# Kernel optimization log

Hardware: AMD Instinct MI355X
Metric: run time of the kernel (lower is better)

Reference implementation:

```python
import jax, jax.numpy as jnp
import numpy as np

IN_F = 2048
OUT_F = 2048
BATCH = 16384
BASE_SPARSITY = 0.02
REVIVAL_DENSITY = 0.2   # rows for dead ('low') output neurons
RELIEF_DENSITY = 0.15   # cols for saturated ('high') input neurons
DEAD = np.arange(16)                      # 'low' extrema (row indices)
SATURATED = np.arange(100, 900, 100)      # 'high' extrema (col indices)


def _make_mask(key):
    k1, k2, k3 = jax.random.split(key, 3)
    base = (jax.random.uniform(k1, (OUT_F, IN_F)) < BASE_SPARSITY).astype(jnp.float32)
    patch = jnp.zeros((OUT_F, IN_F), jnp.float32)
    # dense-ish rows for dead output neurons
    row_patch = (jax.random.uniform(k2, (len(DEAD), IN_F)) < REVIVAL_DENSITY).astype(jnp.float32)
    patch = patch.at[jnp.asarray(DEAD), :].set(row_patch)
    # dense-ish cols for saturated input neurons (overwrite, matching torch order)
    col_patch = (jax.random.uniform(k3, (OUT_F, len(SATURATED))) < RELIEF_DENSITY).astype(jnp.float32)
    patch = patch.at[:, jnp.asarray(SATURATED)].set(col_patch)
    return jnp.maximum(base, patch)


def setup_inputs() -> dict:
    key = jax.random.key(0)
    kx, kw, km = jax.random.split(key, 3)
    x = jax.random.normal(kx, (BATCH, IN_F), dtype=jnp.float32)
    # kaiming_uniform_(a=sqrt(5)) -> U(-bound, bound), bound = sqrt(6/((1+a^2)*fan_in)) = 1/sqrt(fan_in)
    bound = 1.0 / np.sqrt(IN_F)
    weight = jax.random.uniform(kw, (OUT_F, IN_F), minval=-bound, maxval=bound, dtype=jnp.float32)
    bias = jnp.zeros((OUT_F,), jnp.float32)
    mask = _make_mask(km)
    return {"x": x, "weight": weight, "bias": bias, "mask": mask}


def reference(x, weight, bias, mask):
    # F.linear(x, weight * mask, bias): y = x @ (W*M)^T + b
    return jnp.einsum('bi,oi->bo', x, weight * mask) + bias
```

## Files before the change

### kernel.cpp

```cpp
#include <hip/hip_runtime.h>
#include <stdint.h>

#define BATCH 16384
#define IN_F 2048
#define OUT_F 2048

typedef unsigned short u16;
typedef __attribute__((ext_vector_type(8))) short bf16x8;
typedef __attribute__((ext_vector_type(4))) float f32x4;

__device__ __forceinline__ u16 f2bf(float f) {
  union { float f; uint32_t u; } v; v.f = f;
  uint32_t u = v.u;
  u += 0x7FFFu + ((u >> 16) & 1u);
  return (u16)(u >> 16);
}


__global__ void cvt_fused(const float4* __restrict__ x, const float4* __restrict__ w,
                          const float4* __restrict__ m, u16* __restrict__ xb,
                          u16* __restrict__ wb) {
  const int NX = BATCH * IN_F / 4;
  int i = blockIdx.x * 256 + threadIdx.x;
  if (i < NX) {
    float4 v = x[i];
    uint2 p;
    p.x = (uint32_t)f2bf(v.x) | ((uint32_t)f2bf(v.y) << 16);
    p.y = (uint32_t)f2bf(v.z) | ((uint32_t)f2bf(v.w) << 16);
    ((uint2*)xb)[i] = p;
  } else {
    int j = i - NX;
    float4 wv = w[j];
    float4 mv = m[j];
    uint2 p;
    p.x = (uint32_t)f2bf(wv.x * mv.x) | ((uint32_t)f2bf(wv.y * mv.y) << 16);
    p.y = (uint32_t)f2bf(wv.z * mv.z) | ((uint32_t)f2bf(wv.w * mv.w) << 16);
    ((uint2*)wb)[j] = p;
  }
}


__device__ __forceinline__ void async_cp16(const void* g, void* l) {
  __builtin_amdgcn_global_load_lds(
      (const __attribute__((address_space(1))) void*)g,
      (__attribute__((address_space(3))) void*)l,
      16, 0, 0);
}


#define BK 32
#define NT (IN_F / BK)

__global__ __launch_bounds__(512, 2) void gemm_bf16(const u16* __restrict__ A,
                                                    const u16* __restrict__ B,
                                                    const float* __restrict__ bias,
                                                    float* __restrict__ C) {
  __shared__ __align__(128) char smem[4 * 32768];
  const int K = IN_F, N = OUT_F;
  const int tid = threadIdx.x;
  const int lane = tid & 63, wave = tid >> 6;
  const int wm = wave >> 2;
  const int wn = wave & 3;
  const long bn = (long)blockIdx.x * 256;
  const long bm = (long)blockIdx.y * 256;

  const int sr = tid >> 2, sc = tid & 3;
  const int scs = sc ^ ((sr >> 1) & 3);
  const u16* gA = A + (bm + sr) * K + scs * 8;
  const u16* gB = B + (bn + sr) * K + scs * 8;
  const long hiK = 128L * K;
  const int ldst = tid * 16;

  auto stageA = [&](int slot, int kt) {
    char* sb = smem + slot * 32768;
    const long ko = (long)kt * BK;
    async_cp16(gA + ko, sb + ldst);
    async_cp16(gA + hiK + ko, sb + 8192 + ldst);
  };
  auto stageB = [&](int slot, int kt) {
    char* sb = smem + slot * 32768 + 16384;
    const long ko = (long)kt * BK;
    async_cp16(gB + ko, sb + ldst);
    async_cp16(gB + hiK + ko, sb + 8192 + ldst);
  };

  const int rl = lane & 15;
  const int q = lane >> 4;
  const int fb = rl * 64 + ((q ^ ((rl >> 1) & 3)) * 16);
  const int aoff = wm * 8192;
  const int boff = 16384 + wn * 4096;

#define LDA(SLOT, I, HALF) \
  (*(const bf16x8*)(smem + (SLOT) * 32768 + aoff + (HALF) * 4096 + (I) * 1024 + fb))
#define LDB(SLOT, J) \
  (*(const bf16x8*)(smem + (SLOT) * 32768 + boff + (J) * 1024 + fb))

  f32x4 acc[8][4];
#pragma unroll
  for (int i = 0; i < 8; i++)
#pragma unroll
    for (int j = 0; j < 4; j++)
#pragma unroll
      for (int r = 0; r < 4; r++) acc[i][j][r] = 0.0f;

  stageA(0, 0); stageB(0, 0);
  stageA(1, 1); stageB(1, 1);
  stageA(2, 2); stageB(2, 2);
  asm volatile("s_waitcnt vmcnt(4)" ::: "memory");
  __builtin_amdgcn_s_barrier();

  bf16x8 afA[4], bfA[4], afB[4], bfB[4];
#pragma unroll
  for (int i = 0; i < 4; i++) afA[i] = LDA(0, i, 0);
#pragma unroll
  for (int j = 0; j < 4; j++) bfA[j] = LDB(0, j);

#define BODY(T, SLOT, curA, curB, nxtA, nxtB)                                    \
  do {                                                                           \
    const int t_ = (T);                                                          \
    const int kt3_ = (t_ + 3 < NT) ? (t_ + 3) : (NT - 1);                        \
    stageA(((SLOT) + 3) & 3, kt3_);                                              \
    stageB(((SLOT) + 3) & 3, kt3_);                                              \
    bf16x8 af1_[4];                                                              \
    _Pragma("unroll")                                                            \
    for (int i = 0; i < 4; i++) af1_[i] = LDA(SLOT, i, 1);                       \
    __builtin_amdgcn_s_setprio(1);                                               \
    _Pragma("unroll")                                                            \
    for (int i = 0; i < 4; i++)                                                  \
      _Pragma("unroll")                                                          \
      for (int j = 0; j < 4; j++)                                                \
        acc[i][j] = __builtin_amdgcn_mfma_f32_16x16x32_bf16(                     \
            curA[i], curB[j], acc[i][j], 0, 0, 0);                               \
    __builtin_amdgcn_s_setprio(0);                                               \
    _Pragma("unroll")                                                            \
    for (int i = 0; i < 4; i++) nxtA[i] = LDA(((SLOT) + 1) & 3, i, 0);           \
    _Pragma("unroll")                                                            \
    for (int j = 0; j < 4; j++) nxtB[j] = LDB(((SLOT) + 1) & 3, j);              \
    __builtin_amdgcn_s_setprio(1);                                               \
    _Pragma("unroll")                                                            \
    for (int i = 0; i < 4; i++)                                                  \
      _Pragma("unroll")                                                          \
      for (int j = 0; j < 4; j++)                                                \
        acc[4 + i][j] = __builtin_amdgcn_mfma_f32_16x16x32_bf16(                 \
            af1_[i], curB[j], acc[4 + i][j], 0, 0, 0);                           \
    __builtin_amdgcn_s_setprio(0);                                               \
    asm volatile("s_waitcnt vmcnt(4)" ::: "memory");                             \
    __builtin_amdgcn_s_barrier();                                                \
  } while (0)

  for (int t = 0; t < NT; t += 4) {
    BODY(t + 0, 0, afA, bfA, afB, bfB);
    BODY(t + 1, 1, afB, bfB, afA, bfA);
    BODY(t + 2, 2, afA, bfA, afB, bfB);
    BODY(t + 3, 3, afB, bfB, afA, bfA);
  }
#undef BODY
#undef LDA
#undef LDB

  asm volatile("s_waitcnt vmcnt(0)" ::: "memory");

  const int cn = lane & 15;
  const int crow = (lane >> 4) * 4;
#pragma unroll
  for (int j = 0; j < 4; j++) {
    const long n = bn + wn * 64 + j * 16 + cn;
    const float bv = bias[n];
#pragma unroll
    for (int i = 0; i < 8; i++) {
      const long m0 = bm + wm * 128 + i * 16 + crow;
      float* cp = C + m0 * N + n;
#pragma unroll
      for (int r = 0; r < 4; r++)
        cp[(long)r * N] = acc[i][j][r] + bv;
    }
  }
}


__global__ void naive_kernel(const float* __restrict__ x, const float* __restrict__ w,
                             const float* __restrict__ bias, const float* __restrict__ m,
                             float* __restrict__ out) {
  size_t idx = (size_t)blockIdx.x * 256 + threadIdx.x;
  int o = (int)(idx % OUT_F);
  size_t b = idx / OUT_F;
  float s = bias[o];
  const float* xr = x + b * IN_F;
  const float* wr = w + (size_t)o * IN_F;
  const float* mr = m + (size_t)o * IN_F;
  for (int k = 0; k < IN_F; k++) s += xr[k] * wr[k] * mr[k];
  out[idx] = s;
}

extern "C" void kernel_launch(void* const* d_in, const int* in_sizes, int n_in,
                              void* d_out, int out_size, void* d_ws, size_t ws_size,
                              hipStream_t stream) {
  const float* x = (const float*)d_in[0];
  const float* w = (const float*)d_in[1];
  const float* bias = (const float*)d_in[2];
  const float* mask = (const float*)d_in[3];
  float* out = (float*)d_out;

  const size_t xb_elems = (size_t)BATCH * IN_F;
  const size_t wm_elems = (size_t)OUT_F * IN_F;
  const size_t need = (xb_elems + wm_elems) * sizeof(u16);

  if (ws_size >= need) {
    u16* xb = (u16*)d_ws;
    u16* wm = xb + xb_elems;
    const uint32_t nblk = (uint32_t)((xb_elems + wm_elems) / 4 / 256);
    cvt_fused<<<nblk, 256, 0, stream>>>((const float4*)x, (const float4*)w,
                                        (const float4*)mask, xb, wm);
    gemm_bf16<<<dim3(OUT_F / 256, BATCH / 256), 512, 0, stream>>>(xb, wm, bias, out);
  } else {
    naive_kernel<<<(uint32_t)(((size_t)BATCH * OUT_F) / 256), 256, 0, stream>>>(x, w, bias, mask, out);
  }
}
```

Before: 362.8 us.

## Restructure GEMM main loop into barrier-synchronized ping-pong phases without register prefetch

Replaces the register double-buffered loop, which prefetched the next tile's LDS fragments during MFMA, with a per-tile schedule. Each tile now loads its own fragments, issues async global-to-LDS copies split between the two halves, and separates LDS reads from MFMA bursts with extra s_barriers, lgkmcnt waits and sched_barriers. The intent is to lower register pressure and interleave memory and compute phases across waves, ping-pong style. The cost is four barriers per k-tile instead of one, and no overlap of LDS reads with this wave's own MFMAs.

```diff
diff --git a/kernel.cpp b/kernel.cpp
--- a/kernel.cpp
+++ b/kernel.cpp
@@ -109,52 +109,55 @@
   asm volatile("s_waitcnt vmcnt(4)" ::: "memory");
   __builtin_amdgcn_s_barrier();
 
-  bf16x8 afA[4], bfA[4], afB[4], bfB[4];
-#pragma unroll
-  for (int i = 0; i < 4; i++) afA[i] = LDA(0, i, 0);
-#pragma unroll
-  for (int j = 0; j < 4; j++) bfA[j] = LDB(0, j);
-
-#define BODY(T, SLOT, curA, curB, nxtA, nxtB)                                    \
+#define TILE(T, SLOT)                                                            \
   do {                                                                           \
     const int t_ = (T);                                                          \
     const int kt3_ = (t_ + 3 < NT) ? (t_ + 3) : (NT - 1);                        \
+                              \
+    bf16x8 af0_[4], bf_[4], af1_[4];                                             \
+    _Pragma("unroll")                                                            \
+    for (int i = 0; i < 4; i++) af0_[i] = LDA(SLOT, i, 0);                       \
+    _Pragma("unroll")                                                            \
+    for (int j = 0; j < 4; j++) bf_[j] = LDB(SLOT, j);                           \
     stageA(((SLOT) + 3) & 3, kt3_);                                              \
-    stageB(((SLOT) + 3) & 3, kt3_);                                              \
-    bf16x8 af1_[4];                                                              \
-    _Pragma("unroll")                                                            \
-    for (int i = 0; i < 4; i++) af1_[i] = LDA(SLOT, i, 1);                       \
+    __builtin_amdgcn_s_barrier();                                                \
+    asm volatile("s_waitcnt lgkmcnt(0)" ::: "memory");                           \
+    __builtin_amdgcn_sched_barrier(0);                                           \
     __builtin_amdgcn_s_setprio(1);                                               \
     _Pragma("unroll")                                                            \
     for (int i = 0; i < 4; i++)                                                  \
       _Pragma("unroll")                                                          \
       for (int j = 0; j < 4; j++)                                                \
         acc[i][j] = __builtin_amdgcn_mfma_f32_16x16x32_bf16(                     \
-            curA[i], curB[j], acc[i][j], 0, 0, 0);                               \
+            af0_[i], bf_[j], acc[i][j], 0, 0, 0);                                \
     __builtin_amdgcn_s_setprio(0);                                               \
-    _Pragma("unroll")                                                            \
-    for (int i = 0; i < 4; i++) nxtA[i] = LDA(((SLOT) + 1) & 3, i, 0);           \
-    _Pragma("unroll")                                                            \
-    for (int j = 0; j < 4; j++) nxtB[j] = LDB(((SLOT) + 1) & 3, j);              \
+    __builtin_amdgcn_s_barrier();                                                \
+                   \
+    _Pragma("unroll")                                                            \
+    for (int i = 0; i < 4; i++) af1_[i] = LDA(SLOT, i, 1);                       \
+    stageB(((SLOT) + 3) & 3, kt3_);                                              \
+    asm volatile("s_waitcnt vmcnt(4)" ::: "memory");                             \
+    __builtin_amdgcn_s_barrier();                                                \
+    asm volatile("s_waitcnt lgkmcnt(0)" ::: "memory");                           \
+    __builtin_amdgcn_sched_barrier(0);                                           \
     __builtin_amdgcn_s_setprio(1);                                               \
     _Pragma("unroll")                                                            \
     for (int i = 0; i < 4; i++)                                                  \
       _Pragma("unroll")                                                          \
       for (int j = 0; j < 4; j++)                                                \
         acc[4 + i][j] = __builtin_amdgcn_mfma_f32_16x16x32_bf16(                 \
-            af1_[i], curB[j], acc[4 + i][j], 0, 0, 0);                           \
+            af1_[i], bf_[j], acc[4 + i][j], 0, 0, 0);                            \
     __builtin_amdgcn_s_setprio(0);                                               \
-    asm volatile("s_waitcnt vmcnt(4)" ::: "memory");                             \
     __builtin_amdgcn_s_barrier();                                                \
   } while (0)
 
   for (int t = 0; t < NT; t += 4) {
-    BODY(t + 0, 0, afA, bfA, afB, bfB);
-    BODY(t + 1, 1, afB, bfB, afA, bfA);
-    BODY(t + 2, 2, afA, bfA, afB, bfB);
-    BODY(t + 3, 3, afB, bfB, afA, bfA);
-  }
-#undef BODY
+    TILE(t + 0, 0);
+    TILE(t + 1, 1);
+    TILE(t + 2, 2);
+    TILE(t + 3, 3);
+  }
+#undef TILE
 #undef LDA
 #undef LDB
 
```

Result: slower. 374.6 us (+3.3%).
